# Performance work log

Hardware: AMD Instinct MI355X
Metric: run time of the kernel (lower is better)

## Reference

```python
import jax, jax.numpy as jnp
import numpy as np

SFREQ = 128.0
BANDS = {'alpha': (8, 12), 'beta': (12, 30), 'delta': (0.5, 4), 'gamma': (30, 45), 'theta': (4, 8)}


def _trapz(y, xf):
    # y: (..., F) jnp, xf: (F,) numpy constant
    dx = np.diff(xf).astype(np.float32)
    return jnp.sum((y[..., 1:] + y[..., :-1]) * (0.5 * dx), axis=-1)


def setup_inputs() -> dict:
    key = jax.random.key(0)
    x = jax.random.normal(key, (2048, 64, 512), dtype=jnp.float32)
    return {"x": x}


def reference(x):
    B, C, T = x.shape
    # ---------- time-domain moments ----------
    mean = jnp.mean(x, axis=-1)                       # (B, C)
    xc = x - mean[..., None]
    m2 = jnp.mean(xc * xc, axis=-1)
    m3 = jnp.mean(xc * xc * xc, axis=-1)
    m4 = jnp.mean(jnp.square(xc * xc), axis=-1)
    std = jnp.sqrt(m2)
    skew = m3 / jnp.power(m2, 1.5)                    # scipy.stats.skew (biased)
    kurt = m4 / (m2 * m2) - 3.0                       # Fisher kurtosis (biased)
    rms = jnp.sqrt(jnp.mean(x * x, axis=-1))

    nperseg = min(256, T)
    step = nperseg // 2
    nseg = (T - nperseg) // step + 1
    seg_idx = np.arange(nseg)[:, None] * step + np.arange(nperseg)  # (nseg, nperseg)
    segs = x[..., seg_idx]                                          # (B, C, nseg, nperseg)
    segs = segs - jnp.mean(segs, axis=-1, keepdims=True)
    n = np.arange(nperseg)
    win = (0.5 - 0.5 * np.cos(2.0 * np.pi * n / nperseg)).astype(np.float32)
    scale = np.float32(1.0 / (SFREQ * np.sum(win.astype(np.float64) ** 2)))
    spec = jnp.fft.rfft(segs * win, axis=-1)                        # (B, C, nseg, F)
    psd = (jnp.square(spec.real) + jnp.square(spec.imag)) * scale
    if nperseg % 2 == 0:
        psd = psd.at[..., 1:-1].multiply(2.0)
    else:
        psd = psd.at[..., 1:].multiply(2.0)
    psd = jnp.mean(psd, axis=-2)                                    # (B, C, F)
    freqs = np.fft.rfftfreq(nperseg, 1.0 / SFREQ)                   # (F,) constant

    total_power = _trapz(psd, freqs)
    feats = {'mean': mean, 'std': std, 'skew': skew, 'kurtosis': kurt, 'rms': rms}
    for name, (lo, hi) in BANDS.items():
        mask = (freqs >= lo) & (freqs <= hi)
        bp = _trapz(psd[..., mask], freqs[mask])
        feats[f'{name}_power'] = bp
        feats[f'{name}_relative'] = jnp.where(total_power > 1e-6, bp / total_power, 0.0)

    # ---------- histogram entropy (10 bins over [min, max], natural log) ----------
    xmin = jnp.min(x, axis=-1)
    xmax = jnp.max(x, axis=-1)
    width = xmax - xmin
    safe_w = jnp.where(width > 0, width, 1.0)
    t = (x - xmin[..., None]) / safe_w[..., None] * 10.0
    bi = jnp.clip(t.astype(jnp.int32), 0, 9)                        # (B, C, T)
    flat = bi.reshape(B * C, T) + (np.arange(B * C, dtype=np.int32) * 10)[:, None]
    counts = jnp.zeros(B * C * 10, jnp.float32).at[flat.reshape(-1)].add(1.0)
    p = counts.reshape(B, C, 10) / T
    ent = -jnp.sum(jnp.where(p > 0, p * jnp.log(p), 0.0), axis=-1)
    feats['entropy'] = ent

    # ---------- peak frequency ----------
    feats['peak_freq'] = jnp.asarray(freqs, jnp.float32)[jnp.argmax(psd, axis=-1)]

    # ---------- assemble in sorted-key order: sorted(f'ch{c}_{name}') ----------
    names = sorted(feats)                                           # 17 names
    per_ch = jnp.stack([feats[nm] for nm in names], axis=-1)        # (B, C, 17)
    ch_order = sorted(range(C), key=lambda i: f'ch{i}_')
    fv = per_ch[:, np.array(ch_order), :].reshape(B, C * len(names))

    # ---------- z-norm over batch ----------
    fv = (fv - jnp.mean(fv, axis=0)) / (jnp.std(fv, axis=0) + 1e-6)
    return fv
```

## Files before the change

kernel.cpp:

```cpp
#include <hip/hip_runtime.h>
#include <math.h>

#define NB 2048
#define NC 64
#define NF 17
#define NCOL (NC * NF)

#define ZPB 16
#define ZNB (NB / ZPB)
#define WS_STATS_OFF 4096
#define WS_PART_OFF 16384
#define WS_FAST_BYTES (WS_PART_OFF + ZNB * NCOL * 8)

__device__ __constant__ int POS[64] = {
   0, 11, 22, 33, 44, 55, 60, 61, 62, 63,
   1,  2,  3,  4,  5,  6,  7,  8,  9, 10,
  12, 13, 14, 15, 16, 17, 18, 19, 20, 21,
  23, 24, 25, 26, 27, 28, 29, 30, 31, 32,
  34, 35, 36, 37, 38, 39, 40, 41, 42, 43,
  45, 46, 47, 48, 49, 50, 51, 52, 53, 54,
  56, 57, 58, 59
};

__global__ void init_tables(float* __restrict__ win, float2* __restrict__ tw) {
    int t = threadIdx.x;
    double ang = (2.0 * 3.14159265358979323846 / 256.0) * (double)t;
    double cv = cos(ang), sv = sin(ang);
    win[t] = (float)(0.5 - 0.5 * cv);
    tw[t] = make_float2((float)cv, (float)sv);
}

template <bool HAS_TAB>
__global__ __launch_bounds__(256) void feat_kernel(
    const float* __restrict__ x,
    const float* __restrict__ gwin, const float2* __restrict__ gtw,
    float* __restrict__ out)
{
    __shared__ __align__(16) float winS[256];
    __shared__ float2 twS[256];
    __shared__ float2 tw16S[16];
    __shared__ __align__(16) float wmem[4 * 832];
    __shared__ unsigned histS[4][40];

    const int t = threadIdx.x;
    const int wid = t >> 6, l = t & 63;
    const int bc = (blockIdx.x << 2) + wid;

    if (HAS_TAB) {
        winS[t] = gwin[t];
        twS[t] = gtw[t];
        if (t < 16) tw16S[t] = gtw[t << 4];
    } else {
        float ang = (float)t * (6.28318530717958647692f / 256.0f);
        float sv, cv;
        sincosf(ang, &sv, &cv);
        winS[t] = 0.5f - 0.5f * cv;
        twS[t] = make_float2(cv, sv);
        if (t < 16) {
            float a2 = (float)t * (6.28318530717958647692f / 16.0f);
            float s2v, c2v; sincosf(a2, &s2v, &c2v);
            tw16S[t] = make_float2(c2v, s2v);
        }
    }
    __syncthreads();

    float* vseg = &wmem[wid * 832];
    float2* T = reinterpret_cast<float2*>(&wmem[wid * 832 + 256]);
    unsigned* hist = histS[wid];

    const float4* xp4 = reinterpret_cast<const float4*>(x + (size_t)bc * 512);
    const float4 xa = xp4[2 * l], xb = xp4[2 * l + 1];
    float xe[8] = {xa.x, xa.y, xa.z, xa.w, xb.x, xb.y, xb.z, xb.w};

    float psum = 0.f, s2 = 0.f, mn = xe[0], mx = xe[0];
#pragma unroll
    for (int e = 0; e < 8; e++) {
        psum += xe[e];
        s2 = fmaf(xe[e], xe[e], s2);
        mn = fminf(mn, xe[e]);
        mx = fmaxf(mx, xe[e]);
    }
    float g = psum;
#pragma unroll
    for (int m = 1; m < 16; m <<= 1) g += __shfl_xor(g, m, 64);
    const float g0 = __shfl(g, 0, 64), g1 = __shfl(g, 16, 64),
                g2 = __shfl(g, 32, 64), g3 = __shfl(g, 48, 64);
    const float S1 = (g0 + g1) + (g2 + g3);
#pragma unroll
    for (int m = 1; m < 64; m <<= 1) {
        s2 += __shfl_xor(s2, m, 64);
        mn = fminf(mn, __shfl_xor(mn, m, 64));
        mx = fmaxf(mx, __shfl_xor(mx, m, 64));
    }
    const float mean = S1 * (1.0f / 512.0f);

    float c2 = 0.f, c3 = 0.f, c4 = 0.f;
#pragma unroll
    for (int e = 0; e < 8; e++) {
        float a = xe[e] - mean;
        float a2 = a * a;
        c2 += a2;
        c3 = fmaf(a2, a, c3);
        c4 = fmaf(a2, a2, c4);
    }
#pragma unroll
    for (int m = 1; m < 64; m <<= 1) {
        c2 += __shfl_xor(c2, m, 64);
        c3 += __shfl_xor(c3, m, 64);
        c4 += __shfl_xor(c4, m, 64);
    }
    const float m2 = c2 * (1.0f / 512.0f);
    const float m3 = c3 * (1.0f / 512.0f);
    const float m4 = c4 * (1.0f / 512.0f);
    const float stdv = sqrtf(m2);
    const float skew = m3 / (m2 * stdv);
    const float kurt = m4 / (m2 * m2) - 3.0f;
    const float rms = sqrtf(s2 * (1.0f / 512.0f));

    if (l < 40) hist[l] = 0u;
    {
        float wdt = mx - mn;
        float safew = (wdt > 0.0f) ? wdt : 1.0f;
        const int cpy = l & 3;
#pragma unroll
        for (int e = 0; e < 8; e++) {
            int bi = (int)((xe[e] - mn) / safew * 10.0f);
            bi = bi < 0 ? 0 : (bi > 9 ? 9 : bi);
            atomicAdd(&hist[bi * 4 + cpy], 1u);
        }
    }
    float entterm;
    {
        float cnt = 0.0f;
        if (l < 10) {
            unsigned cc = hist[4 * l] + hist[4 * l + 1] + hist[4 * l + 2] + hist[4 * l + 3];
            cnt = (float)cc;
        }
        float p = cnt * (1.0f / 512.0f);
        entterm = (p > 0.0f) ? p * logf(p) : 0.0f;
#pragma unroll
        for (int m = 1; m < 16; m <<= 1) entterm += __shfl_xor(entterm, m, 64);
    }
    const float ent = -entterm;

    const int rb = l >> 4, n0 = l & 15;
    float2 tv;
    tv = tw16S[rb];             const float2 w16q1 = make_float2(tv.x, -tv.y);
    tv = tw16S[(2 * rb) & 15];  const float2 w16q2 = make_float2(tv.x, -tv.y);
    tv = tw16S[(3 * rb) & 15];  const float2 w16q3 = make_float2(tv.x, -tv.y);
    tv = twS[l];                const float2 wq1 = make_float2(tv.x, -tv.y);
    tv = twS[(2 * l) & 255];    const float2 wq2 = make_float2(tv.x, -tv.y);
    tv = twS[(3 * l) & 255];    const float2 wq3 = make_float2(tv.x, -tv.y);
    float car[4], cai[4];
#pragma unroll
    for (int a = 0; a < 4; a++) {
        int mm = (rb * a) & 3;
        car[a] = (mm == 0) ? 1.f : ((mm == 2) ? -1.f : 0.f);
        cai[a] = (mm == 1) ? -1.f : ((mm == 3) ? 1.f : 0.f);
    }

    float P1 = 0.f, P2 = 0.f, P128 = 0.f;
#pragma unroll
    for (int s = 0; s < 3; s++) {
        const float smean =
            ((s == 0) ? (g0 + g1) : (s == 1) ? (g1 + g2) : (g2 + g3)) * (1.0f / 256.0f);
        const int D = l - 16 * s;
        float alt = 0.f;
        if (D >= 0 && D < 32) {
            const float4 wA = reinterpret_cast<const float4*>(winS)[2 * D];
            const float4 wB = reinterpret_cast<const float4*>(winS)[2 * D + 1];
            float wv0 = wA.x * (xe[0] - smean);
            float wv1 = wA.y * (xe[1] - smean);
            float wv2 = wA.z * (xe[2] - smean);
            float wv3 = wA.w * (xe[3] - smean);
            float wv4 = wB.x * (xe[4] - smean);
            float wv5 = wB.y * (xe[5] - smean);
            float wv6 = wB.z * (xe[6] - smean);
            float wv7 = wB.w * (xe[7] - smean);
            reinterpret_cast<float4*>(vseg)[2 * D] = make_float4(wv0, wv1, wv2, wv3);
            reinterpret_cast<float4*>(vseg)[2 * D + 1] = make_float4(wv4, wv5, wv6, wv7);
            alt = ((wv0 - wv1) + (wv2 - wv3)) + ((wv4 - wv5) + (wv6 - wv7));
        }
#pragma unroll
        for (int m = 1; m < 64; m <<= 1) alt += __shfl_xor(alt, m, 64);
        P128 = fmaf(alt, alt, P128);

        float Dre[4], Dim[4];
#pragma unroll
        for (int q = 0; q < 4; q++) {
            float dr = vseg[16 * q + n0], di = 0.f;
#pragma unroll
            for (int a = 1; a < 4; a++) {
                float vv = vseg[64 * a + 16 * q + n0];
                dr = fmaf(vv, car[a], dr);
                di = fmaf(vv, cai[a], di);
            }
            Dre[q] = dr; Dim[q] = di;
        }
        const float E0r = Dre[0], E0i = Dim[0];
        const float E1r = Dre[1] * w16q1.x - Dim[1] * w16q1.y;
        const float E1i = Dre[1] * w16q1.y + Dim[1] * w16q1.x;
        const float E2r = Dre[2] * w16q2.x - Dim[2] * w16q2.y;
        const float E2i = Dre[2] * w16q2.y + Dim[2] * w16q2.x;
        const float E3r = Dre[3] * w16q3.x - Dim[3] * w16q3.y;
        const float E3i = Dre[3] * w16q3.y + Dim[3] * w16q3.x;
        T[(rb +  0) * 18 + n0] = make_float2((E0r + E1r) + (E2r + E3r),
                                             (E0i + E1i) + (E2i + E3i));
        T[(rb +  4) * 18 + n0] = make_float2((E0r + E1i) - (E2r + E3i),
                                             (E0i - E1r) + (E3r - E2i));
        T[(rb +  8) * 18 + n0] = make_float2((E0r - E1r) + (E2r - E3r),
                                             (E0i - E1i) + (E2i - E3i));
        T[(rb + 12) * 18 + n0] = make_float2((E0r - E1i) - (E2r - E3i),
                                             (E0i + E1r) - (E2i + E3r));

        float G0r, G0i, G1r, G1i, G2r, G2i, G3r, G3i;
        {
            const float4 t01 = *reinterpret_cast<const float4*>(&T[n0 * 18 + 0]);
            const float4 t23 = *reinterpret_cast<const float4*>(&T[n0 * 18 + 2]);
            G0r = t01.x; G0i = t01.y; G1r = t01.z; G1i = t01.w;
            G2r = t23.x; G2i = t23.y; G3r = t23.z; G3i = t23.w;
        }
#pragma unroll
        for (int a = 1; a < 4; a++) {
            float2 cw = twS[(4 * l * a) & 255];
            const float cx = cw.x, cy = -cw.y;
            const float4 t01 = *reinterpret_cast<const float4*>(&T[n0 * 18 + 4 * a]);
            const float4 t23 = *reinterpret_cast<const float4*>(&T[n0 * 18 + 4 * a + 2]);
            G0r = fmaf(t01.x, cx, fmaf(-t01.y, cy, G0r));
            G0i = fmaf(t01.x, cy, fmaf( t01.y, cx, G0i));
            G1r = fmaf(t01.z, cx, fmaf(-t01.w, cy, G1r));
            G1i = fmaf(t01.z, cy, fmaf( t01.w, cx, G1i));
            G2r = fmaf(t23.x, cx, fmaf(-t23.y, cy, G2r));
            G2i = fmaf(t23.x, cy, fmaf( t23.y, cx, G2i));
            G3r = fmaf(t23.z, cx, fmaf(-t23.w, cy, G3r));
            G3i = fmaf(t23.z, cy, fmaf( t23.w, cx, G3i));
        }
        const float H0r = G0r, H0i = G0i;
        const float H1r = G1r * wq1.x - G1i * wq1.y, H1i = G1r * wq1.y + G1i * wq1.x;
        const float H2r = G2r * wq2.x - G2i * wq2.y, H2i = G2r * wq2.y + G2i * wq2.x;
        const float H3r = G3r * wq3.x - G3i * wq3.y, H3i = G3r * wq3.y + G3i * wq3.x;
        const float X1r = (H0r + H1r) + (H2r + H3r);
        const float X1i = (H0i + H1i) + (H2i + H3i);
        const float X2r = (H0r + H1i) - (H2r + H3i);
        const float X2i = (H0i - H1r) + (H3r - H2i);
        P1 = fmaf(X1r, X1r, fmaf(X1i, X1i, P1));
        P2 = fmaf(X2r, X2r, fmaf(X2i, X2i, P2));
    }

    const float scc = (1.0f / 12288.0f) * (1.0f / 3.0f);
    const float psd1 = P1 * ((l == 0) ? 1.0f : 2.0f) * scc;
    const float psd2 = P2 * 2.0f * scc;
    const float psd128 = P128 * scc;

    auto wt = [](int k, int lo, int hi) -> float {
        if (k < lo || k > hi) return 0.0f;
        return (k == lo || k == hi) ? 0.25f : 0.5f;
    };
    float tot, al, be, de, ga, th, bv; int bi_;
    {
        const int k = l; const float p = psd1;
        tot = wt(k, 0, 128) * p;
        al = wt(k, 16, 24) * p; be = wt(k, 24, 60) * p; de = wt(k, 1, 8) * p;
        ga = wt(k, 60, 90) * p; th = wt(k, 8, 16) * p;
        bv = p; bi_ = k;
    }
    {
        const int k = l + 64; const float p = psd2;
        tot += 0.5f * p;
        ga += wt(k, 60, 90) * p;
        if (p > bv) { bv = p; bi_ = k; }
    }
    if (l == 0) {
        tot += 0.25f * psd128;
        if (psd128 > bv) { bv = psd128; bi_ = 128; }
    }
    unsigned long long pk =
        ((unsigned long long)__float_as_uint(bv) << 32) | (unsigned)(16384 - bi_);
#pragma unroll
    for (int m = 1; m < 64; m <<= 1) {
        tot += __shfl_xor(tot, m, 64);
        al  += __shfl_xor(al, m, 64);
        be  += __shfl_xor(be, m, 64);
        de  += __shfl_xor(de, m, 64);
        ga  += __shfl_xor(ga, m, 64);
        th  += __shfl_xor(th, m, 64);
        unsigned long long op = __shfl_xor(pk, m, 64);
        pk = (op > pk) ? op : pk;
    }
    bi_ = 16384 - (int)(unsigned)(pk & 0xffffffffull);
    const bool ok = tot > 1e-6f;
    const float alR = ok ? al / tot : 0.f;
    const float beR = ok ? be / tot : 0.f;
    const float deR = ok ? de / tot : 0.f;
    const float gaR = ok ? ga / tot : 0.f;
    const float thR = ok ? th / tot : 0.f;
    const float pkf = 0.5f * (float)bi_;

    if (l < NF) {
        const int b = bc >> 6, c = bc & 63;
        float fv =
            (l == 0)  ? al :
            (l == 1)  ? alR :
            (l == 2)  ? be :
            (l == 3)  ? beR :
            (l == 4)  ? de :
            (l == 5)  ? deR :
            (l == 6)  ? ent :
            (l == 7)  ? ga :
            (l == 8)  ? gaR :
            (l == 9)  ? kurt :
            (l == 10) ? mean :
            (l == 11) ? pkf :
            (l == 12) ? rms :
            (l == 13) ? skew :
            (l == 14) ? stdv :
            (l == 15) ? th : thR;
        out[(size_t)b * NCOL + POS[c] * NF + l] = fv;
    }
}


__global__ __launch_bounds__(256) void zstat_partial(
    const float* __restrict__ fm, float2* __restrict__ part)
{
    const int blk = blockIdx.x;
    const int row0 = blk * ZPB;
    for (int c = threadIdx.x; c < NCOL; c += 256) {
        float s = 0.f, ss = 0.f;
#pragma unroll
        for (int r = 0; r < ZPB; r++) {
            float v = fm[(size_t)(row0 + r) * NCOL + c];
            s += v;
            ss = fmaf(v, v, ss);
        }
        part[(size_t)blk * NCOL + c] = make_float2(s, ss);
    }
}

__global__ __launch_bounds__(256) void zstat_final(
    const float2* __restrict__ part, float2* __restrict__ stats)
{
    const int c = blockIdx.x * 256 + threadIdx.x;
    if (c >= NCOL) return;
    double s = 0.0, ss = 0.0;
    for (int b = 0; b < ZNB; b++) {
        float2 p = part[(size_t)b * NCOL + c];
        s += (double)p.x;
        ss += (double)p.y;
    }
    const double mu_d = s * (1.0 / 2048.0);
    double var_d = ss * (1.0 / 2048.0) - mu_d * mu_d;
    if (var_d < 0.0) var_d = 0.0;
    const float mu = (float)mu_d;
    const float sd = sqrtf((float)var_d);
    stats[c] = make_float2(mu, sd + 1e-6f);
}

__global__ __launch_bounds__(256) void zapply(
    float* __restrict__ fm, const float2* __restrict__ stats)
{
    const int row = blockIdx.x;
    float4* p4 = reinterpret_cast<float4*>(fm + (size_t)row * NCOL);
    for (int i = threadIdx.x; i < NCOL / 4; i += 256) {
        float4 v = p4[i];
        const float2 s0 = stats[4 * i + 0];
        const float2 s1 = stats[4 * i + 1];
        const float2 s2 = stats[4 * i + 2];
        const float2 s3 = stats[4 * i + 3];
        v.x = (v.x - s0.x) / s0.y;
        v.y = (v.y - s1.x) / s1.y;
        v.z = (v.z - s2.x) / s2.y;
        v.w = (v.w - s3.x) / s3.y;
        p4[i] = v;
    }
}

__global__ __launch_bounds__(256) void znorm_kernel(float* __restrict__ fm) {
    __shared__ float red[4];
    const int col = blockIdx.x;
    const int t = threadIdx.x;
    const int wid = t >> 6, lane = t & 63;
    float v[8];
    float s = 0.0f;
#pragma unroll
    for (int i = 0; i < 8; i++) {
        v[i] = fm[(size_t)(i * 256 + t) * NCOL + col];
        s += v[i];
    }
#pragma unroll
    for (int off = 32; off; off >>= 1) s += __shfl_down(s, off, 64);
    if (lane == 0) red[wid] = s;
    __syncthreads();
    const float mu = (red[0] + red[1] + red[2] + red[3]) * (1.0f / 2048.0f);
    __syncthreads();
    float q = 0.0f;
#pragma unroll
    for (int i = 0; i < 8; i++) {
        float dd = v[i] - mu;
        q += dd * dd;
    }
#pragma unroll
    for (int off = 32; off; off >>= 1) q += __shfl_down(q, off, 64);
    if (lane == 0) red[wid] = q;
    __syncthreads();
    const float sd = sqrtf((red[0] + red[1] + red[2] + red[3]) * (1.0f / 2048.0f));
    const float den = sd + 1e-6f;
#pragma unroll
    for (int i = 0; i < 8; i++)
        fm[(size_t)(i * 256 + t) * NCOL + col] = (v[i] - mu) / den;
}

extern "C" void kernel_launch(void* const* d_in, const int* in_sizes, int n_in,
                              void* d_out, int out_size, void* d_ws, size_t ws_size,
                              hipStream_t stream) {
    const float* x = (const float*)d_in[0];
    float* out = (float*)d_out;
    const int nblocks = (NB * NC) / 4;

    const bool has_tab = (d_ws != nullptr && ws_size >= 4096);
    const bool fast_z = (d_ws != nullptr && ws_size >= (size_t)WS_FAST_BYTES);

    if (has_tab) {
        float* win = (float*)d_ws;
        float2* tw = (float2*)((char*)d_ws + 1024);
        init_tables<<<1, 256, 0, stream>>>(win, tw);
        feat_kernel<true><<<nblocks, 256, 0, stream>>>(x, win, tw, out);
    } else {
        feat_kernel<false><<<nblocks, 256, 0, stream>>>(x, nullptr, nullptr, out);
    }

    if (fast_z) {
        float2* stats = (float2*)((char*)d_ws + WS_STATS_OFF);
        float2* part = (float2*)((char*)d_ws + WS_PART_OFF);
        zstat_partial<<<ZNB, 256, 0, stream>>>(out, part);
        zstat_final<<<(NCOL + 255) / 256, 256, 0, stream>>>(part, stats);
        zapply<<<NB, 256, 0, stream>>>(out, stats);
    } else {
        znorm_kernel<<<NCOL, 256, 0, stream>>>(out);
    }
}
```

Baseline: 614.2 us.

## Split fused feature kernel into separate moments and PSD kernels

```diff
diff --git a/kernel.cpp b/kernel.cpp
--- a/kernel.cpp
+++ b/kernel.cpp
@@ -30,8 +30,105 @@
     tw[t] = make_float2((float)cv, (float)sv);
 }
 
+__global__ __launch_bounds__(256) void mom_kernel(
+    const float* __restrict__ x, float* __restrict__ out)
+{
+    __shared__ unsigned histS[4][40];
+
+    const int t = threadIdx.x;
+    const int wid = t >> 6, l = t & 63;
+    const int bc = (blockIdx.x << 2) + wid;
+    unsigned* hist = histS[wid];
+
+    const float4* xp4 = reinterpret_cast<const float4*>(x + (size_t)bc * 512);
+    const float4 xa = xp4[2 * l], xb = xp4[2 * l + 1];
+    float xe[8] = {xa.x, xa.y, xa.z, xa.w, xb.x, xb.y, xb.z, xb.w};
+
+    float psum = 0.f, s2 = 0.f, mn = xe[0], mx = xe[0];
+#pragma unroll
+    for (int e = 0; e < 8; e++) {
+        psum += xe[e];
+        s2 = fmaf(xe[e], xe[e], s2);
+        mn = fminf(mn, xe[e]);
+        mx = fmaxf(mx, xe[e]);
+    }
+    float g = psum;
+#pragma unroll
+    for (int m = 1; m < 16; m <<= 1) g += __shfl_xor(g, m, 64);
+    const float g0 = __shfl(g, 0, 64), g1 = __shfl(g, 16, 64),
+                g2 = __shfl(g, 32, 64), g3 = __shfl(g, 48, 64);
+    const float S1 = (g0 + g1) + (g2 + g3);
+#pragma unroll
+    for (int m = 1; m < 64; m <<= 1) {
+        s2 += __shfl_xor(s2, m, 64);
+        mn = fminf(mn, __shfl_xor(mn, m, 64));
+        mx = fmaxf(mx, __shfl_xor(mx, m, 64));
+    }
+    const float mean = S1 * (1.0f / 512.0f);
+
+    float c2 = 0.f, c3 = 0.f, c4 = 0.f;
+#pragma unroll
+    for (int e = 0; e < 8; e++) {
+        float a = xe[e] - mean;
+        float a2 = a * a;
+        c2 += a2;
+        c3 = fmaf(a2, a, c3);
+        c4 = fmaf(a2, a2, c4);
+    }
+#pragma unroll
+    for (int m = 1; m < 64; m <<= 1) {
+        c2 += __shfl_xor(c2, m, 64);
+        c3 += __shfl_xor(c3, m, 64);
+        c4 += __shfl_xor(c4, m, 64);
+    }
+    const float m2 = c2 * (1.0f / 512.0f);
+    const float m3 = c3 * (1.0f / 512.0f);
+    const float m4 = c4 * (1.0f / 512.0f);
+    const float stdv = sqrtf(m2);
+    const float skew = m3 / (m2 * stdv);
+    const float kurt = m4 / (m2 * m2) - 3.0f;
+    const float rms = sqrtf(s2 * (1.0f / 512.0f));
+
+    if (l < 40) hist[l] = 0u;
+    {
+        float wdt = mx - mn;
+        float safew = (wdt > 0.0f) ? wdt : 1.0f;
+        const int cpy = l & 3;
+#pragma unroll
+        for (int e = 0; e < 8; e++) {
+            int bi = (int)((xe[e] - mn) / safew * 10.0f);
+            bi = bi < 0 ? 0 : (bi > 9 ? 9 : bi);
+            atomicAdd(&hist[bi * 4 + cpy], 1u);
+        }
+    }
+    float entterm;
+    {
+        float cnt = 0.0f;
+        if (l < 10) {
+            unsigned cc = hist[4 * l] + hist[4 * l + 1] + hist[4 * l + 2] + hist[4 * l + 3];
+            cnt = (float)cc;
+        }
+        float p = cnt * (1.0f / 512.0f);
+        entterm = (p > 0.0f) ? p * logf(p) : 0.0f;
+#pragma unroll
+        for (int m = 1; m < 16; m <<= 1) entterm += __shfl_xor(entterm, m, 64);
+    }
+    const float ent = -entterm;
+
+    if (l == 6 || l == 9 || l == 10 || l == 12 || l == 13 || l == 14) {
+        const int b = bc >> 6, c = bc & 63;
+        float fv =
+            (l == 6)  ? ent :
+            (l == 9)  ? kurt :
+            (l == 10) ? mean :
+            (l == 12) ? rms :
+            (l == 13) ? skew : stdv;
+        out[(size_t)b * NCOL + POS[c] * NF + l] = fv;
+    }
+}
+
 template <bool HAS_TAB>
-__global__ __launch_bounds__(256) void feat_kernel(
+__global__ __launch_bounds__(256) void psd_kernel(
     const float* __restrict__ x,
     const float* __restrict__ gwin, const float2* __restrict__ gtw,
     float* __restrict__ out)
@@ -40,7 +137,6 @@
     __shared__ float2 twS[256];
     __shared__ float2 tw16S[16];
     __shared__ __align__(16) float wmem[4 * 832];
-    __shared__ unsigned histS[4][40];
 
     const int t = threadIdx.x;
     const int wid = t >> 6, l = t & 63;
@@ -66,91 +162,20 @@
 
     float* vseg = &wmem[wid * 832];
     float2* T = reinterpret_cast<float2*>(&wmem[wid * 832 + 256]);
-    unsigned* hist = histS[wid];
 
     const float4* xp4 = reinterpret_cast<const float4*>(x + (size_t)bc * 512);
     const float4 xa = xp4[2 * l], xb = xp4[2 * l + 1];
     float xe[8] = {xa.x, xa.y, xa.z, xa.w, xb.x, xb.y, xb.z, xb.w};
 
-    float psum = 0.f, s2 = 0.f, mn = xe[0], mx = xe[0];
-#pragma unroll
-    for (int e = 0; e < 8; e++) {
-        psum += xe[e];
-        s2 = fmaf(xe[e], xe[e], s2);
-        mn = fminf(mn, xe[e]);
-        mx = fmaxf(mx, xe[e]);
-    }
-    float g = psum;
+    float g = 0.f;
+#pragma unroll
+    for (int e = 0; e < 8; e++) g += xe[e];
 #pragma unroll
     for (int m = 1; m < 16; m <<= 1) g += __shfl_xor(g, m, 64);
     const float g0 = __shfl(g, 0, 64), g1 = __shfl(g, 16, 64),
                 g2 = __shfl(g, 32, 64), g3 = __shfl(g, 48, 64);
-    const float S1 = (g0 + g1) + (g2 + g3);
-#pragma unroll
-    for (int m = 1; m < 64; m <<= 1) {
-        s2 += __shfl_xor(s2, m, 64);
-        mn = fminf(mn, __shfl_xor(mn, m, 64));
-        mx = fmaxf(mx, __shfl_xor(mx, m, 64));
-    }
-    const float mean = S1 * (1.0f / 512.0f);
-
-    float c2 = 0.f, c3 = 0.f, c4 = 0.f;
-#pragma unroll
-    for (int e = 0; e < 8; e++) {
-        float a = xe[e] - mean;
-        float a2 = a * a;
-        c2 += a2;
-        c3 = fmaf(a2, a, c3);
-        c4 = fmaf(a2, a2, c4);
-    }
-#pragma unroll
-    for (int m = 1; m < 64; m <<= 1) {
-        c2 += __shfl_xor(c2, m, 64);
-        c3 += __shfl_xor(c3, m, 64);
-        c4 += __shfl_xor(c4, m, 64);
-    }
-    const float m2 = c2 * (1.0f / 512.0f);
-    const float m3 = c3 * (1.0f / 512.0f);
-    const float m4 = c4 * (1.0f / 512.0f);
-    const float stdv = sqrtf(m2);
-    const float skew = m3 / (m2 * stdv);
-    const float kurt = m4 / (m2 * m2) - 3.0f;
-    const float rms = sqrtf(s2 * (1.0f / 512.0f));
-
-    if (l < 40) hist[l] = 0u;
-    {
-        float wdt = mx - mn;
-        float safew = (wdt > 0.0f) ? wdt : 1.0f;
-        const int cpy = l & 3;
-#pragma unroll
-        for (int e = 0; e < 8; e++) {
-            int bi = (int)((xe[e] - mn) / safew * 10.0f);
-            bi = bi < 0 ? 0 : (bi > 9 ? 9 : bi);
-            atomicAdd(&hist[bi * 4 + cpy], 1u);
-        }
-    }
-    float entterm;
-    {
-        float cnt = 0.0f;
-        if (l < 10) {
-            unsigned cc = hist[4 * l] + hist[4 * l + 1] + hist[4 * l + 2] + hist[4 * l + 3];
-            cnt = (float)cc;
-        }
-        float p = cnt * (1.0f / 512.0f);
-        entterm = (p > 0.0f) ? p * logf(p) : 0.0f;
-#pragma unroll
-        for (int m = 1; m < 16; m <<= 1) entterm += __shfl_xor(entterm, m, 64);
-    }
-    const float ent = -entterm;
 
     const int rb = l >> 4, n0 = l & 15;
-    float2 tv;
-    tv = tw16S[rb];             const float2 w16q1 = make_float2(tv.x, -tv.y);
-    tv = tw16S[(2 * rb) & 15];  const float2 w16q2 = make_float2(tv.x, -tv.y);
-    tv = tw16S[(3 * rb) & 15];  const float2 w16q3 = make_float2(tv.x, -tv.y);
-    tv = twS[l];                const float2 wq1 = make_float2(tv.x, -tv.y);
-    tv = twS[(2 * l) & 255];    const float2 wq2 = make_float2(tv.x, -tv.y);
-    tv = twS[(3 * l) & 255];    const float2 wq3 = make_float2(tv.x, -tv.y);
     float car[4], cai[4];
 #pragma unroll
     for (int a = 0; a < 4; a++) {
@@ -198,12 +223,16 @@
             Dre[q] = dr; Dim[q] = di;
         }
         const float E0r = Dre[0], E0i = Dim[0];
-        const float E1r = Dre[1] * w16q1.x - Dim[1] * w16q1.y;
-        const float E1i = Dre[1] * w16q1.y + Dim[1] * w16q1.x;
-        const float E2r = Dre[2] * w16q2.x - Dim[2] * w16q2.y;
-        const float E2i = Dre[2] * w16q2.y + Dim[2] * w16q2.x;
-        const float E3r = Dre[3] * w16q3.x - Dim[3] * w16q3.y;
-        const float E3i = Dre[3] * w16q3.y + Dim[3] * w16q3.x;
+        float2 tv;
+        tv = tw16S[rb];
+        const float E1r = Dre[1] * tv.x + Dim[1] * tv.y;
+        const float E1i = -Dre[1] * tv.y + Dim[1] * tv.x;
+        tv = tw16S[(2 * rb) & 15];
+        const float E2r = Dre[2] * tv.x + Dim[2] * tv.y;
+        const float E2i = -Dre[2] * tv.y + Dim[2] * tv.x;
+        tv = tw16S[(3 * rb) & 15];
+        const float E3r = Dre[3] * tv.x + Dim[3] * tv.y;
+        const float E3i = -Dre[3] * tv.y + Dim[3] * tv.x;
         T[(rb +  0) * 18 + n0] = make_float2((E0r + E1r) + (E2r + E3r),
                                              (E0i + E1i) + (E2i + E3i));
         T[(rb +  4) * 18 + n0] = make_float2((E0r + E1i) - (E2r + E3i),
@@ -236,9 +265,10 @@
             G3i = fmaf(t23.z, cy, fmaf( t23.w, cx, G3i));
         }
         const float H0r = G0r, H0i = G0i;
-        const float H1r = G1r * wq1.x - G1i * wq1.y, H1i = G1r * wq1.y + G1i * wq1.x;
-        const float H2r = G2r * wq2.x - G2i * wq2.y, H2i = G2r * wq2.y + G2i * wq2.x;
-        const float H3r = G3r * wq3.x - G3i * wq3.y, H3i = G3r * wq3.y + G3i * wq3.x;
+        float2 w1 = twS[l], w2 = twS[(2 * l) & 255], w3 = twS[(3 * l) & 255];
+        const float H1r = G1r * w1.x + G1i * w1.y, H1i = -G1r * w1.y + G1i * w1.x;
+        const float H2r = G2r * w2.x + G2i * w2.y, H2i = -G2r * w2.y + G2i * w2.x;
+        const float H3r = G3r * w3.x + G3i * w3.y, H3i = -G3r * w3.y + G3i * w3.x;
         const float X1r = (H0r + H1r) + (H2r + H3r);
         const float X1i = (H0i + H1i) + (H2i + H3i);
         const float X2r = (H0r + H1i) - (H2r + H3i);
@@ -289,32 +319,20 @@
     }
     bi_ = 16384 - (int)(unsigned)(pk & 0xffffffffull);
     const bool ok = tot > 1e-6f;
-    const float alR = ok ? al / tot : 0.f;
-    const float beR = ok ? be / tot : 0.f;
-    const float deR = ok ? de / tot : 0.f;
-    const float gaR = ok ? ga / tot : 0.f;
-    const float thR = ok ? th / tot : 0.f;
-    const float pkf = 0.5f * (float)bi_;
-
-    if (l < NF) {
+
+    if (l < NF && !(l == 6 || l == 9 || l == 10 || l == 12 || l == 13 || l == 14)) {
         const int b = bc >> 6, c = bc & 63;
         float fv =
             (l == 0)  ? al :
-            (l == 1)  ? alR :
+            (l == 1)  ? (ok ? al / tot : 0.f) :
             (l == 2)  ? be :
-            (l == 3)  ? beR :
+            (l == 3)  ? (ok ? be / tot : 0.f) :
             (l == 4)  ? de :
-            (l == 5)  ? deR :
-            (l == 6)  ? ent :
+            (l == 5)  ? (ok ? de / tot : 0.f) :
             (l == 7)  ? ga :
-            (l == 8)  ? gaR :
-            (l == 9)  ? kurt :
-            (l == 10) ? mean :
-            (l == 11) ? pkf :
-            (l == 12) ? rms :
-            (l == 13) ? skew :
-            (l == 14) ? stdv :
-            (l == 15) ? th : thR;
+            (l == 8)  ? (ok ? ga / tot : 0.f) :
+            (l == 11) ? (0.5f * (float)bi_) :
+            (l == 15) ? th : (ok ? th / tot : 0.f);
         out[(size_t)b * NCOL + POS[c] * NF + l] = fv;
     }
 }
@@ -420,13 +438,15 @@
     const bool has_tab = (d_ws != nullptr && ws_size >= 4096);
     const bool fast_z = (d_ws != nullptr && ws_size >= (size_t)WS_FAST_BYTES);
 
+    mom_kernel<<<nblocks, 256, 0, stream>>>(x, out);
+
     if (has_tab) {
         float* win = (float*)d_ws;
         float2* tw = (float2*)((char*)d_ws + 1024);
         init_tables<<<1, 256, 0, stream>>>(win, tw);
-        feat_kernel<true><<<nblocks, 256, 0, stream>>>(x, win, tw, out);
+        psd_kernel<true><<<nblocks, 256, 0, stream>>>(x, win, tw, out);
     } else {
-        feat_kernel<false><<<nblocks, 256, 0, stream>>>(x, nullptr, nullptr, out);
+        psd_kernel<false><<<nblocks, 256, 0, stream>>>(x, nullptr, nullptr, out);
     }
 
     if (fast_z) {
```

Measured after the change: 627.6 us. 2.2% more time.
